# Kernel tuning notes

Hardware: AMD Instinct MI355X
Metric: run time of the kernel (lower is better)

Reference implementation:

```python
import jax, jax.numpy as jnp
import numpy as np

T_LEN, E_LEN, BATCH, DIM = 32, 256, 16, 512  # topic_len, exp_len, batch, input=hidden size
HID = 512


def setup_inputs() -> dict:
    key = jax.random.key(0)
    k1, k2, k3, k4, k5, k6 = jax.random.split(key, 6)
    topic = jax.random.normal(k1, (T_LEN, BATCH, DIM), dtype=jnp.float32)
    exp_output = jax.random.normal(k2, (E_LEN, BATCH, DIM), dtype=jnp.float32)
    seq_mask = jax.random.bernoulli(k3, 0.1, (E_LEN, BATCH))  # True = masked exp position
    # nn.Linear(hidden+input, hidden): weight [HID, HID+DIM], bias [HID]
    lim1 = 1.0 / np.sqrt(HID + DIM)
    W_attn = jax.random.uniform(k4, (HID, HID + DIM), minval=-lim1, maxval=lim1, dtype=jnp.float32)
    b_attn = jax.random.uniform(k5, (HID,), minval=-lim1, maxval=lim1, dtype=jnp.float32)
    # nn.Linear(hidden, 1): weight [1, HID], bias [1]
    lim2 = 1.0 / np.sqrt(HID)
    kv, kb = jax.random.split(k6)
    v_score = jax.random.uniform(kv, (1, HID), minval=-lim2, maxval=lim2, dtype=jnp.float32)
    b_score = jax.random.uniform(kb, (1,), minval=-lim2, maxval=lim2, dtype=jnp.float32)
    return {"topic": topic, "exp_output": exp_output, "seq_mask": seq_mask,
            "W_attn": W_attn, "b_attn": b_attn, "v_score": v_score, "b_score": b_score}


def reference(topic, exp_output, seq_mask, W_attn, b_attn, v_score, b_score):
    # topic: [T, B, D]; exp_output: [E, B, D]; seq_mask: [E, B] bool
    D = topic.shape[2]
    # Split the concat-Linear: cat(topic, exp) @ W.T == topic @ W[:, :D].T + exp @ W[:, D:].T
    proj_t = jnp.einsum('tbd,hd->bth', topic, W_attn[:, :D])        # [B, T, H]
    proj_e = jnp.einsum('ebd,hd->beh', exp_output, W_attn[:, D:])   # [B, E, H]
    feat = jnp.tanh(proj_t[:, :, None, :] + proj_e[:, None, :, :] + b_attn)  # [B, T, E, H]
    energies = jnp.einsum('bteh,h->bte', feat, v_score[0]) + b_score[0]      # [B, T, E]
    # mask exp positions (broadcast over topic dim), as masked_fill(-1e12)
    energies = jnp.where(seq_mask.T[:, None, :], jnp.float32(-1e12), energies)
    attn_s1 = jax.nn.softmax(jnp.swapaxes(energies, 1, 2), axis=2)  # [B, E, T], softmax over topics
    attn_s2 = jax.nn.softmax(energies, axis=2)                      # [B, T, E], softmax over exp
    new_exp = jnp.einsum('bet,btd->bed', attn_s1, jnp.swapaxes(topic, 0, 1))       # [B, E, D]
    new_topic = jnp.einsum('bte,bed->btd', attn_s2, jnp.swapaxes(exp_output, 0, 1))  # [B, T, D]
    return new_topic, new_exp
```

## Files before the change

### kernel.cpp

```cpp
#include <hip/hip_runtime.h>
#include <hip/hip_bf16.h>
#include <cstddef>
#include <cstdint>

#define T_LEN 32
#define E_LEN 256
#define BATCH 16
#define DIM 512
#define HID 512
#define WROW 1024

#define TWO_LOG2E 2.8853900817779268f
#define LOG2E 1.4426950408889634f

typedef __attribute__((ext_vector_type(8))) short bf16x8;
typedef __attribute__((ext_vector_type(4))) float f32x4;

__device__ inline bf16x8 cvt8(float4 a, float4 b) {
    union { bf16x8 v; __hip_bfloat16 h[8]; } u;
    u.h[0] = __float2bfloat16(a.x); u.h[1] = __float2bfloat16(a.y);
    u.h[2] = __float2bfloat16(a.z); u.h[3] = __float2bfloat16(a.w);
    u.h[4] = __float2bfloat16(b.x); u.h[5] = __float2bfloat16(b.y);
    u.h[6] = __float2bfloat16(b.z); u.h[7] = __float2bfloat16(b.w);
    return u.v;
}

#define GPAD 8
#define GLDR (64 + GPAD)

__global__ __launch_bounds__(256) void gemm_fused_k(
    const float* __restrict__ topic, const float* __restrict__ expo,
    const float* __restrict__ W, const float* __restrict__ battn,
    float* __restrict__ EPT, __hip_bfloat16* __restrict__ EPE) {
    __shared__ __align__(16) __hip_bfloat16 As[2][64 * GLDR];
    __shared__ __align__(16) __hip_bfloat16 Bs[2][64 * GLDR];
    const int tid = threadIdx.x;
    const int by = blockIdx.x >> 3;
    const int n0 = (blockIdx.x & 7) * 64;
    const float* A; const float* Wp; int m0;
    const bool isT = (by < 8);
    if (isT) { A = topic; Wp = W;       m0 = by * 64; }
    else     { A = expo;  Wp = W + DIM; m0 = (by - 8) * 64; }
    const int w = tid >> 6;
    const int lane = tid & 63;
    const int l15 = lane & 15;
    const int g = lane >> 4;
    const int srow = tid >> 2;
    const int sc = tid & 3;

    f32x4 acc[4];
    const f32x4 z = {0.f, 0.f, 0.f, 0.f};
#pragma unroll
    for (int nt = 0; nt < 4; ++nt) acc[nt] = z;

    const float* ga = A + (size_t)(m0 + srow) * 512 + sc * 8;
    const float* gb = Wp + (size_t)(n0 + srow) * WROW + sc * 8;

    float4 a0 = *(const float4*)(ga);
    float4 a1 = *(const float4*)(ga + 4);
    float4 a2 = *(const float4*)(ga + 32);
    float4 a3 = *(const float4*)(ga + 36);
    float4 b0 = *(const float4*)(gb);
    float4 b1 = *(const float4*)(gb + 4);
    float4 b2 = *(const float4*)(gb + 32);
    float4 b3 = *(const float4*)(gb + 36);

    for (int kk = 0; kk < 8; ++kk) {
        const int cur = kk & 1;
        bf16x8 av0 = cvt8(a0, a1), av1 = cvt8(a2, a3);
        bf16x8 bv0 = cvt8(b0, b1), bv1 = cvt8(b2, b3);
        if (kk < 7) {
            ga += 64; gb += 64;
            a0 = *(const float4*)(ga);
            a1 = *(const float4*)(ga + 4);
            a2 = *(const float4*)(ga + 32);
            a3 = *(const float4*)(ga + 36);
            b0 = *(const float4*)(gb);
            b1 = *(const float4*)(gb + 4);
            b2 = *(const float4*)(gb + 32);
            b3 = *(const float4*)(gb + 36);
        }
        *(bf16x8*)&As[cur][srow * GLDR + sc * 8] = av0;
        *(bf16x8*)&As[cur][srow * GLDR + sc * 8 + 32] = av1;
        *(bf16x8*)&Bs[cur][srow * GLDR + sc * 8] = bv0;
        *(bf16x8*)&Bs[cur][srow * GLDR + sc * 8 + 32] = bv1;
        __syncthreads();
#pragma unroll
        for (int s = 0; s < 2; ++s) {
            bf16x8 af = *(const bf16x8*)&As[cur][(w * 16 + l15) * GLDR + (s * 4 + g) * 8];
#pragma unroll
            for (int nt = 0; nt < 4; ++nt) {
                bf16x8 bf = *(const bf16x8*)&Bs[cur][(nt * 16 + l15) * GLDR + (s * 4 + g) * 8];
                acc[nt] = __builtin_amdgcn_mfma_f32_16x16x32_bf16(af, bf, acc[nt], 0, 0, 0);
            }
        }
    }
    if (isT) {
#pragma unroll
        for (int nt = 0; nt < 4; ++nt) {
            int n = n0 + nt * 16 + l15;
            float bv = battn[n];
#pragma unroll
            for (int r = 0; r < 4; ++r) {
                int m = m0 + w * 16 + g * 4 + r;
                EPT[(size_t)m * 512 + n] =
                    __builtin_amdgcn_exp2f((acc[nt][r] + bv) * TWO_LOG2E);
            }
        }
    } else {
#pragma unroll
        for (int nt = 0; nt < 4; ++nt) {
            int n = n0 + nt * 16 + l15;
#pragma unroll
            for (int r = 0; r < 4; ++r) {
                int m = m0 + w * 16 + g * 4 + r;
                EPE[(size_t)m * 512 + n] = __float2bfloat16(
                    __builtin_amdgcn_exp2f(acc[nt][r] * TWO_LOG2E));
            }
        }
    }
}

__global__ __launch_bounds__(256) void energies_k(
    const float* __restrict__ EPT, const __hip_bfloat16* __restrict__ EPE,
    const float* __restrict__ v, const int* __restrict__ mask,
    float* __restrict__ P, float* __restrict__ PT) {
    const int u = blockIdx.x;
    const int b = u & 15;
    const int tg = (u >> 4) & 3;
    const int ech = u >> 6;
    const int tid = threadIdx.x;
    const int lane = tid & 63;
    const int w = tid >> 6;
    const int h0 = lane * 8;
    const int e0 = ech * 16 + w * 4;
    const bool o1 = (lane & 1) != 0;
    const bool o2 = (lane & 2) != 0;
    const bool o4 = (lane & 4) != 0;

    int mk[4];
#pragma unroll
    for (int ei = 0; ei < 4; ++ei) mk[ei] = mask[(e0 + ei) * BATCH + b];

    float sv[8], sv2[4], spt[8][8];
    {
        float4 v0 = *(const float4*)(v + h0);
        float4 v1 = *(const float4*)(v + h0 + 4);
        sv[0] = -2.f * v0.x; sv[1] = -2.f * v0.y; sv[2] = -2.f * v0.z; sv[3] = -2.f * v0.w;
        sv[4] = -2.f * v1.x; sv[5] = -2.f * v1.y; sv[6] = -2.f * v1.z; sv[7] = -2.f * v1.w;
        sv2[0] = sv[0] + sv[1]; sv2[1] = sv[2] + sv[3];
        sv2[2] = sv[4] + sv[5]; sv2[3] = sv[6] + sv[7];
#pragma unroll
        for (int i = 0; i < 8; ++i) {
            const float* p = EPT + ((size_t)((tg * 8 + i) * BATCH + b)) * HID + h0;
            float4 p0 = *(const float4*)(p);
            float4 p1 = *(const float4*)(p + 4);
            spt[i][0] = p0.x; spt[i][1] = p0.y; spt[i][2] = p0.z; spt[i][3] = p0.w;
            spt[i][4] = p1.x; spt[i][5] = p1.y; spt[i][6] = p1.z; spt[i][7] = p1.w;
        }
    }
#pragma unroll
    for (int ei = 0; ei < 4; ++ei) {
        const int e = e0 + ei;
        if (mk[ei] != 0) {
            if (lane < 8) {
                P[((size_t)b * T_LEN + tg * 8 + lane) * E_LEN + e] = 1e-30f;
                PT[((size_t)b * E_LEN + e) * T_LEN + tg * 8 + lane] = 1e-30f;
            }
            continue;
        }
        union { bf16x8 v8; __hip_bfloat16 h[8]; } pv;
        pv.v8 = *(const bf16x8*)(EPE + ((size_t)(e * BATCH + b)) * HID + h0);
        float pr[8];
#pragma unroll
        for (int j = 0; j < 8; ++j) pr[j] = __bfloat162float(pv.h[j]);
        float a[8] = {0.f, 0.f, 0.f, 0.f, 0.f, 0.f, 0.f, 0.f};
#pragma unroll
        for (int i = 0; i < 8; ++i) {
#pragma unroll
            for (int jq = 0; jq < 2; ++jq) {
                const int j0 = jq * 4;
                float a0 = spt[i][j0 + 0] * pr[j0 + 0];
                float a1 = spt[i][j0 + 1] * pr[j0 + 1];
                float a2 = spt[i][j0 + 2] * pr[j0 + 2];
                float a3 = spt[i][j0 + 3] * pr[j0 + 3];
                float u0 = a0 + 1.0f;
                float u2 = a2 + 1.0f;
                float d01 = fmaf(a1, u0, u0);
                float d23 = fmaf(a3, u2, u2);
                float n01 = fmaf(sv[j0 + 0], a1, fmaf(sv[j0 + 1], a0, sv2[jq * 2 + 0]));
                float n23 = fmaf(sv[j0 + 2], a3, fmaf(sv[j0 + 3], a2, sv2[jq * 2 + 1]));
                float nn = fmaf(n01, d23, n23 * d01);
                float dd = d01 * d23;
                a[i] = fmaf(nn, __builtin_amdgcn_rcpf(dd), a[i]);
            }
        }
        float s, b0, b1, b2, b3, d0, d1, f;
        s = __shfl_xor(o1 ? a[0] : a[1], 1); b0 = (o1 ? a[1] : a[0]) + s;
        s = __shfl_xor(o1 ? a[2] : a[3], 1); b1 = (o1 ? a[3] : a[2]) + s;
        s = __shfl_xor(o1 ? a[4] : a[5], 1); b2 = (o1 ? a[5] : a[4]) + s;
        s = __shfl_xor(o1 ? a[6] : a[7], 1); b3 = (o1 ? a[7] : a[6]) + s;
        s = __shfl_xor(o2 ? b0 : b1, 2); d0 = (o2 ? b1 : b0) + s;
        s = __shfl_xor(o2 ? b2 : b3, 2); d1 = (o2 ? b3 : b2) + s;
        s = __shfl_xor(o4 ? d0 : d1, 4); f = (o4 ? d1 : d0) + s;
        f += __shfl_xor(f, 8);
        f += __shfl_xor(f, 16);
        f += __shfl_xor(f, 32);
        if (lane < 8) {
            float pe = __builtin_amdgcn_exp2f(f * LOG2E);
            P[((size_t)b * T_LEN + tg * 8 + lane) * E_LEN + e] = pe;
            PT[((size_t)b * E_LEN + e) * T_LEN + tg * 8 + lane] = pe;
        }
    }
}

__global__ __launch_bounds__(256) void epilogue_k(
    const float* __restrict__ P, const float* __restrict__ PT,
    const float* __restrict__ topic,
    const float* __restrict__ expo, float* __restrict__ out) {
    __shared__ __align__(16) float smem[5120];
    const int tid = threadIdx.x;
    const int lane = tid & 63;
    const int w = tid >> 6;
    if (blockIdx.x < 512) {
        const int b = blockIdx.x >> 5;
        const int ech = (blockIdx.x >> 1) & 15;
        const int hf = blockIdx.x & 1;
        const int e0 = ech * 16 + w * 4;
#pragma unroll
        for (int ei = 0; ei < 4; ++ei) {
            const int e = e0 + ei;
            float x = 0.f;
            if (lane < T_LEN)
                x = PT[((size_t)b * E_LEN + e) * T_LEN + lane];
            float s = x;
#pragma unroll
            for (int off = 32; off; off >>= 1) s += __shfl_xor(s, off);
            float wv = x * __builtin_amdgcn_rcpf(s);
            if (lane < T_LEN) smem[(w * 4 + ei) * 32 + lane] = wv;
        }
        __syncthreads();
        const int d0 = hf * 256 + lane * 4;
        float4 acc[4];
#pragma unroll
        for (int ei = 0; ei < 4; ++ei) acc[ei] = {0.f, 0.f, 0.f, 0.f};
#pragma unroll 2
        for (int tq = 0; tq < 8; ++tq) {
            float wqa[4][4];
#pragma unroll
            for (int ei = 0; ei < 4; ++ei) {
                float4 q = *(const float4*)&smem[(w * 4 + ei) * 32 + tq * 4];
                wqa[ei][0] = q.x; wqa[ei][1] = q.y; wqa[ei][2] = q.z; wqa[ei][3] = q.w;
            }
#pragma unroll
            for (int tt = 0; tt < 4; ++tt) {
                const int t = tq * 4 + tt;
                float4 r = *(const float4*)(topic + ((size_t)t * BATCH + b) * DIM + d0);
#pragma unroll
                for (int ei = 0; ei < 4; ++ei) {
                    acc[ei].x = fmaf(wqa[ei][tt], r.x, acc[ei].x);
                    acc[ei].y = fmaf(wqa[ei][tt], r.y, acc[ei].y);
                    acc[ei].z = fmaf(wqa[ei][tt], r.z, acc[ei].z);
                    acc[ei].w = fmaf(wqa[ei][tt], r.w, acc[ei].w);
                }
            }
        }
#pragma unroll
        for (int ei = 0; ei < 4; ++ei) {
            float* o = out + (size_t)BATCH * T_LEN * DIM +
                       ((size_t)b * E_LEN + e0 + ei) * DIM + d0;
            *(float4*)o = acc[ei];
        }
    } else {
        const int q = blockIdx.x - 512;
        const int b = q >> 4;
        const int tq = (q >> 1) & 7;
        const int hf = q & 1;
        {
            const int bt = b * T_LEN + tq * 4 + w;
            float4 xv = *(const float4*)&P[(size_t)bt * E_LEN + lane * 4];
            float s = xv.x + xv.y + xv.z + xv.w;
#pragma unroll
            for (int off = 32; off; off >>= 1) s += __shfl_xor(s, off);
            float inv = __builtin_amdgcn_rcpf(s);
            smem[(lane * 4 + 0) * 4 + w] = xv.x * inv;
            smem[(lane * 4 + 1) * 4 + w] = xv.y * inv;
            smem[(lane * 4 + 2) * 4 + w] = xv.z * inv;
            smem[(lane * 4 + 3) * 4 + w] = xv.w * inv;
        }
        __syncthreads();
        const int dl = lane * 4;
        const int dglob = hf * 256 + dl;
        float4 a0 = {0.f, 0.f, 0.f, 0.f};
        float4 a1 = {0.f, 0.f, 0.f, 0.f};
        float4 a2 = {0.f, 0.f, 0.f, 0.f};
        float4 a3 = {0.f, 0.f, 0.f, 0.f};
        const float* base = expo + (size_t)b * DIM + dglob;
        for (int ee = 0; ee < 64; ++ee) {
            const int e = w * 64 + ee;
            float4 rv = *(const float4*)(base + (size_t)e * BATCH * DIM);
            float4 wq = *(const float4*)&smem[e * 4];
            a0.x = fmaf(wq.x, rv.x, a0.x); a0.y = fmaf(wq.x, rv.y, a0.y);
            a0.z = fmaf(wq.x, rv.z, a0.z); a0.w = fmaf(wq.x, rv.w, a0.w);
            a1.x = fmaf(wq.y, rv.x, a1.x); a1.y = fmaf(wq.y, rv.y, a1.y);
            a1.z = fmaf(wq.y, rv.z, a1.z); a1.w = fmaf(wq.y, rv.w, a1.w);
            a2.x = fmaf(wq.z, rv.x, a2.x); a2.y = fmaf(wq.z, rv.y, a2.y);
            a2.z = fmaf(wq.z, rv.z, a2.z); a2.w = fmaf(wq.z, rv.w, a2.w);
            a3.x = fmaf(wq.w, rv.x, a3.x); a3.y = fmaf(wq.w, rv.y, a3.y);
            a3.z = fmaf(wq.w, rv.z, a3.z); a3.w = fmaf(wq.w, rv.w, a3.w);
        }
        *(float4*)&smem[1024 + (w * 4 + 0) * 256 + dl] = a0;
        *(float4*)&smem[1024 + (w * 4 + 1) * 256 + dl] = a1;
        *(float4*)&smem[1024 + (w * 4 + 2) * 256 + dl] = a2;
        *(float4*)&smem[1024 + (w * 4 + 3) * 256 + dl] = a3;
        __syncthreads();
#pragma unroll
        for (int tt = 0; tt < 4; ++tt) {
            float sum = smem[1024 + (0 * 4 + tt) * 256 + tid] +
                        smem[1024 + (1 * 4 + tt) * 256 + tid] +
                        smem[1024 + (2 * 4 + tt) * 256 + tid] +
                        smem[1024 + (3 * 4 + tt) * 256 + tid];
            out[((size_t)b * T_LEN + tq * 4 + tt) * DIM + hf * 256 + tid] = sum;
        }
    }
}

extern "C" void kernel_launch(void* const* d_in, const int* in_sizes, int n_in,
                              void* d_out, int out_size, void* d_ws, size_t ws_size,
                              hipStream_t stream) {
    const float* topic = (const float*)d_in[0];
    const float* expo  = (const float*)d_in[1];
    const int*   mask  = (const int*)d_in[2];
    const float* W     = (const float*)d_in[3];
    const float* battn = (const float*)d_in[4];
    const float* vsc   = (const float*)d_in[5];
    float* out = (float*)d_out;

    float* EPT = (float*)d_ws;
    __hip_bfloat16* EPE = (__hip_bfloat16*)(EPT + 512 * 512);
    float* P  = (float*)(EPE + (size_t)4096 * 512);
    float* PT = P + (size_t)BATCH * T_LEN * E_LEN;

    gemm_fused_k<<<576, 256, 0, stream>>>(topic, expo, W, battn, EPT, EPE);
    energies_k<<<1024, 256, 0, stream>>>(EPT, EPE, vsc, mask, P, PT);
    epilogue_k<<<768, 256, 0, stream>>>(P, PT, topic, expo, out);
}
```

Before: 111.2 us.

## Fuse topic-softmax and new_exp computation into energies kernel via LDS

The energies kernel now assigns each block all 32 topics for 8 exp positions of one batch, loops over topic chunks, and keeps the exp weights in LDS. It then normalizes over topics and computes new_exp directly, which removes the PT transposed buffer and its global round trip. The new_topic part becomes its own smaller kernel. In exchange the grid drops from 1024 to 512 blocks and EPT rows are reloaded per topic chunk, which may lower parallelism.

```diff
diff --git a/kernel.cpp b/kernel.cpp
--- a/kernel.cpp
+++ b/kernel.cpp
@@ -121,28 +121,29 @@
     }
 }
 
-__global__ __launch_bounds__(256) void energies_k(
+__global__ __launch_bounds__(256) void energies_exp_k(
     const float* __restrict__ EPT, const __hip_bfloat16* __restrict__ EPE,
     const float* __restrict__ v, const int* __restrict__ mask,
-    float* __restrict__ P, float* __restrict__ PT) {
+    const float* __restrict__ topic, float* __restrict__ P,
+    float* __restrict__ out) {
+    __shared__ __align__(16) float P_lds[8][32];
     const int u = blockIdx.x;
-    const int b = u & 15;
-    const int tg = (u >> 4) & 3;
-    const int ech = u >> 6;
+    const int b = u >> 5;
+    const int ech = u & 31;
     const int tid = threadIdx.x;
     const int lane = tid & 63;
     const int w = tid >> 6;
     const int h0 = lane * 8;
-    const int e0 = ech * 16 + w * 4;
+    const int e0 = ech * 8 + w * 2;
     const bool o1 = (lane & 1) != 0;
     const bool o2 = (lane & 2) != 0;
     const bool o4 = (lane & 4) != 0;
 
-    int mk[4];
-#pragma unroll
-    for (int ei = 0; ei < 4; ++ei) mk[ei] = mask[(e0 + ei) * BATCH + b];
-
-    float sv[8], sv2[4], spt[8][8];
+    int mk[2];
+    mk[0] = mask[(e0 + 0) * BATCH + b];
+    mk[1] = mask[(e0 + 1) * BATCH + b];
+
+    float sv[8], sv2[4];
     {
         float4 v0 = *(const float4*)(v + h0);
         float4 v1 = *(const float4*)(v + h0 + 4);
@@ -150,178 +151,183 @@
         sv[4] = -2.f * v1.x; sv[5] = -2.f * v1.y; sv[6] = -2.f * v1.z; sv[7] = -2.f * v1.w;
         sv2[0] = sv[0] + sv[1]; sv2[1] = sv[2] + sv[3];
         sv2[2] = sv[4] + sv[5]; sv2[3] = sv[6] + sv[7];
+    }
+    float pr2[2][8];
+#pragma unroll
+    for (int ei = 0; ei < 2; ++ei) {
+        if (mk[ei] == 0) {
+            union { bf16x8 v8; __hip_bfloat16 h[8]; } pv;
+            pv.v8 = *(const bf16x8*)(EPE + ((size_t)((e0 + ei) * BATCH + b)) * HID + h0);
+#pragma unroll
+            for (int j = 0; j < 8; ++j) pr2[ei][j] = __bfloat162float(pv.h[j]);
+        }
+    }
+
+    for (int tc = 0; tc < 4; ++tc) {
+        float spt[8][8];
 #pragma unroll
         for (int i = 0; i < 8; ++i) {
-            const float* p = EPT + ((size_t)((tg * 8 + i) * BATCH + b)) * HID + h0;
+            const float* p = EPT + ((size_t)((tc * 8 + i) * BATCH + b)) * HID + h0;
             float4 p0 = *(const float4*)(p);
             float4 p1 = *(const float4*)(p + 4);
             spt[i][0] = p0.x; spt[i][1] = p0.y; spt[i][2] = p0.z; spt[i][3] = p0.w;
             spt[i][4] = p1.x; spt[i][5] = p1.y; spt[i][6] = p1.z; spt[i][7] = p1.w;
         }
-    }
-#pragma unroll
-    for (int ei = 0; ei < 4; ++ei) {
-        const int e = e0 + ei;
-        if (mk[ei] != 0) {
+#pragma unroll
+        for (int ei = 0; ei < 2; ++ei) {
+            const int e = e0 + ei;
+            if (mk[ei] != 0) {
+                if (lane < 8) {
+                    P[((size_t)b * T_LEN + tc * 8 + lane) * E_LEN + e] = 1e-30f;
+                    P_lds[w * 2 + ei][tc * 8 + lane] = 1e-30f;
+                }
+                continue;
+            }
+            float a[8] = {0.f, 0.f, 0.f, 0.f, 0.f, 0.f, 0.f, 0.f};
+#pragma unroll
+            for (int i = 0; i < 8; ++i) {
+#pragma unroll
+                for (int jq = 0; jq < 2; ++jq) {
+                    const int j0 = jq * 4;
+                    float a0 = spt[i][j0 + 0] * pr2[ei][j0 + 0];
+                    float a1 = spt[i][j0 + 1] * pr2[ei][j0 + 1];
+                    float a2 = spt[i][j0 + 2] * pr2[ei][j0 + 2];
+                    float a3 = spt[i][j0 + 3] * pr2[ei][j0 + 3];
+                    float u0 = a0 + 1.0f;
+                    float u2 = a2 + 1.0f;
+                    float d01 = fmaf(a1, u0, u0);
+                    float d23 = fmaf(a3, u2, u2);
+                    float n01 = fmaf(sv[j0 + 0], a1, fmaf(sv[j0 + 1], a0, sv2[jq * 2 + 0]));
+                    float n23 = fmaf(sv[j0 + 2], a3, fmaf(sv[j0 + 3], a2, sv2[jq * 2 + 1]));
+                    float nn = fmaf(n01, d23, n23 * d01);
+                    float dd = d01 * d23;
+                    a[i] = fmaf(nn, __builtin_amdgcn_rcpf(dd), a[i]);
+                }
+            }
+            float s, b0, b1, b2, b3, d0, d1, f;
+            s = __shfl_xor(o1 ? a[0] : a[1], 1); b0 = (o1 ? a[1] : a[0]) + s;
+            s = __shfl_xor(o1 ? a[2] : a[3], 1); b1 = (o1 ? a[3] : a[2]) + s;
+            s = __shfl_xor(o1 ? a[4] : a[5], 1); b2 = (o1 ? a[5] : a[4]) + s;
+            s = __shfl_xor(o1 ? a[6] : a[7], 1); b3 = (o1 ? a[7] : a[6]) + s;
+            s = __shfl_xor(o2 ? b0 : b1, 2); d0 = (o2 ? b1 : b0) + s;
+            s = __shfl_xor(o2 ? b2 : b3, 2); d1 = (o2 ? b3 : b2) + s;
+            s = __shfl_xor(o4 ? d0 : d1, 4); f = (o4 ? d1 : d0) + s;
+            f += __shfl_xor(f, 8);
+            f += __shfl_xor(f, 16);
+            f += __shfl_xor(f, 32);
             if (lane < 8) {
-                P[((size_t)b * T_LEN + tg * 8 + lane) * E_LEN + e] = 1e-30f;
-                PT[((size_t)b * E_LEN + e) * T_LEN + tg * 8 + lane] = 1e-30f;
-            }
-            continue;
-        }
-        union { bf16x8 v8; __hip_bfloat16 h[8]; } pv;
-        pv.v8 = *(const bf16x8*)(EPE + ((size_t)(e * BATCH + b)) * HID + h0);
-        float pr[8];
-#pragma unroll
-        for (int j = 0; j < 8; ++j) pr[j] = __bfloat162float(pv.h[j]);
-        float a[8] = {0.f, 0.f, 0.f, 0.f, 0.f, 0.f, 0.f, 0.f};
-#pragma unroll
-        for (int i = 0; i < 8; ++i) {
-#pragma unroll
-            for (int jq = 0; jq < 2; ++jq) {
-                const int j0 = jq * 4;
-                float a0 = spt[i][j0 + 0] * pr[j0 + 0];
-                float a1 = spt[i][j0 + 1] * pr[j0 + 1];
-                float a2 = spt[i][j0 + 2] * pr[j0 + 2];
-                float a3 = spt[i][j0 + 3] * pr[j0 + 3];
-                float u0 = a0 + 1.0f;
-                float u2 = a2 + 1.0f;
-                float d01 = fmaf(a1, u0, u0);
-                float d23 = fmaf(a3, u2, u2);
-                float n01 = fmaf(sv[j0 + 0], a1, fmaf(sv[j0 + 1], a0, sv2[jq * 2 + 0]));
-                float n23 = fmaf(sv[j0 + 2], a3, fmaf(sv[j0 + 3], a2, sv2[jq * 2 + 1]));
-                float nn = fmaf(n01, d23, n23 * d01);
-                float dd = d01 * d23;
-                a[i] = fmaf(nn, __builtin_amdgcn_rcpf(dd), a[i]);
-            }
-        }
-        float s, b0, b1, b2, b3, d0, d1, f;
-        s = __shfl_xor(o1 ? a[0] : a[1], 1); b0 = (o1 ? a[1] : a[0]) + s;
-        s = __shfl_xor(o1 ? a[2] : a[3], 1); b1 = (o1 ? a[3] : a[2]) + s;
-        s = __shfl_xor(o1 ? a[4] : a[5], 1); b2 = (o1 ? a[5] : a[4]) + s;
-        s = __shfl_xor(o1 ? a[6] : a[7], 1); b3 = (o1 ? a[7] : a[6]) + s;
-        s = __shfl_xor(o2 ? b0 : b1, 2); d0 = (o2 ? b1 : b0) + s;
-        s = __shfl_xor(o2 ? b2 : b3, 2); d1 = (o2 ? b3 : b2) + s;
-        s = __shfl_xor(o4 ? d0 : d1, 4); f = (o4 ? d1 : d0) + s;
-        f += __shfl_xor(f, 8);
-        f += __shfl_xor(f, 16);
-        f += __shfl_xor(f, 32);
-        if (lane < 8) {
-            float pe = __builtin_amdgcn_exp2f(f * LOG2E);
-            P[((size_t)b * T_LEN + tg * 8 + lane) * E_LEN + e] = pe;
-            PT[((size_t)b * E_LEN + e) * T_LEN + tg * 8 + lane] = pe;
-        }
-    }
-}
-
-__global__ __launch_bounds__(256) void epilogue_k(
-    const float* __restrict__ P, const float* __restrict__ PT,
-    const float* __restrict__ topic,
-    const float* __restrict__ expo, float* __restrict__ out) {
+                float pe = __builtin_amdgcn_exp2f(f * LOG2E);
+                P[((size_t)b * T_LEN + tc * 8 + lane) * E_LEN + e] = pe;
+                P_lds[w * 2 + ei][tc * 8 + lane] = pe;
+            }
+        }
+    }
+    __syncthreads();
+
+    const int el0 = w * 2, el1 = w * 2 + 1;
+    float s0 = 0.f, s1 = 0.f;
+#pragma unroll
+    for (int q = 0; q < 8; ++q) {
+        float4 x = *(const float4*)&P_lds[el0][q * 4];
+        s0 += (x.x + x.y) + (x.z + x.w);
+        float4 y = *(const float4*)&P_lds[el1][q * 4];
+        s1 += (y.x + y.y) + (y.z + y.w);
+    }
+    const float inv0 = __builtin_amdgcn_rcpf(s0);
+    const float inv1 = __builtin_amdgcn_rcpf(s1);
+
+    const int dA = lane * 4;
+    const int dB = 256 + lane * 4;
+    float4 aA0 = {0.f, 0.f, 0.f, 0.f}, aB0 = {0.f, 0.f, 0.f, 0.f};
+    float4 aA1 = {0.f, 0.f, 0.f, 0.f}, aB1 = {0.f, 0.f, 0.f, 0.f};
+#pragma unroll 2
+    for (int tq = 0; tq < 8; ++tq) {
+        float4 w0 = *(const float4*)&P_lds[el0][tq * 4];
+        float4 w1 = *(const float4*)&P_lds[el1][tq * 4];
+        w0.x *= inv0; w0.y *= inv0; w0.z *= inv0; w0.w *= inv0;
+        w1.x *= inv1; w1.y *= inv1; w1.z *= inv1; w1.w *= inv1;
+        float wt0[4] = {w0.x, w0.y, w0.z, w0.w};
+        float wt1[4] = {w1.x, w1.y, w1.z, w1.w};
+#pragma unroll
+        for (int tt = 0; tt < 4; ++tt) {
+            const int t = tq * 4 + tt;
+            const float* tp = topic + ((size_t)t * BATCH + b) * DIM;
+            float4 rA = *(const float4*)(tp + dA);
+            float4 rB = *(const float4*)(tp + dB);
+            aA0.x = fmaf(wt0[tt], rA.x, aA0.x); aA0.y = fmaf(wt0[tt], rA.y, aA0.y);
+            aA0.z = fmaf(wt0[tt], rA.z, aA0.z); aA0.w = fmaf(wt0[tt], rA.w, aA0.w);
+            aB0.x = fmaf(wt0[tt], rB.x, aB0.x); aB0.y = fmaf(wt0[tt], rB.y, aB0.y);
+            aB0.z = fmaf(wt0[tt], rB.z, aB0.z); aB0.w = fmaf(wt0[tt], rB.w, aB0.w);
+            aA1.x = fmaf(wt1[tt], rA.x, aA1.x); aA1.y = fmaf(wt1[tt], rA.y, aA1.y);
+            aA1.z = fmaf(wt1[tt], rA.z, aA1.z); aA1.w = fmaf(wt1[tt], rA.w, aA1.w);
+            aB1.x = fmaf(wt1[tt], rB.x, aB1.x); aB1.y = fmaf(wt1[tt], rB.y, aB1.y);
+            aB1.z = fmaf(wt1[tt], rB.z, aB1.z); aB1.w = fmaf(wt1[tt], rB.w, aB1.w);
+        }
+    }
+    float* oe0 = out + (size_t)BATCH * T_LEN * DIM + ((size_t)b * E_LEN + e0) * DIM;
+    *(float4*)(oe0 + dA) = aA0;
+    *(float4*)(oe0 + dB) = aB0;
+    float* oe1 = oe0 + DIM;
+    *(float4*)(oe1 + dA) = aA1;
+    *(float4*)(oe1 + dB) = aB1;
+}
+
+__global__ __launch_bounds__(256) void newtopic_k(
+    const float* __restrict__ P, const float* __restrict__ expo,
+    float* __restrict__ out) {
     __shared__ __align__(16) float smem[5120];
     const int tid = threadIdx.x;
     const int lane = tid & 63;
     const int w = tid >> 6;
-    if (blockIdx.x < 512) {
-        const int b = blockIdx.x >> 5;
-        const int ech = (blockIdx.x >> 1) & 15;
-        const int hf = blockIdx.x & 1;
-        const int e0 = ech * 16 + w * 4;
-#pragma unroll
-        for (int ei = 0; ei < 4; ++ei) {
-            const int e = e0 + ei;
-            float x = 0.f;
-            if (lane < T_LEN)
-                x = PT[((size_t)b * E_LEN + e) * T_LEN + lane];
-            float s = x;
-#pragma unroll
-            for (int off = 32; off; off >>= 1) s += __shfl_xor(s, off);
-            float wv = x * __builtin_amdgcn_rcpf(s);
-            if (lane < T_LEN) smem[(w * 4 + ei) * 32 + lane] = wv;
-        }
-        __syncthreads();
-        const int d0 = hf * 256 + lane * 4;
-        float4 acc[4];
-#pragma unroll
-        for (int ei = 0; ei < 4; ++ei) acc[ei] = {0.f, 0.f, 0.f, 0.f};
-#pragma unroll 2
-        for (int tq = 0; tq < 8; ++tq) {
-            float wqa[4][4];
-#pragma unroll
-            for (int ei = 0; ei < 4; ++ei) {
-                float4 q = *(const float4*)&smem[(w * 4 + ei) * 32 + tq * 4];
-                wqa[ei][0] = q.x; wqa[ei][1] = q.y; wqa[ei][2] = q.z; wqa[ei][3] = q.w;
-            }
-#pragma unroll
-            for (int tt = 0; tt < 4; ++tt) {
-                const int t = tq * 4 + tt;
-                float4 r = *(const float4*)(topic + ((size_t)t * BATCH + b) * DIM + d0);
-#pragma unroll
-                for (int ei = 0; ei < 4; ++ei) {
-                    acc[ei].x = fmaf(wqa[ei][tt], r.x, acc[ei].x);
-                    acc[ei].y = fmaf(wqa[ei][tt], r.y, acc[ei].y);
-                    acc[ei].z = fmaf(wqa[ei][tt], r.z, acc[ei].z);
-                    acc[ei].w = fmaf(wqa[ei][tt], r.w, acc[ei].w);
-                }
-            }
-        }
-#pragma unroll
-        for (int ei = 0; ei < 4; ++ei) {
-            float* o = out + (size_t)BATCH * T_LEN * DIM +
-                       ((size_t)b * E_LEN + e0 + ei) * DIM + d0;
-            *(float4*)o = acc[ei];
-        }
-    } else {
-        const int q = blockIdx.x - 512;
-        const int b = q >> 4;
-        const int tq = (q >> 1) & 7;
-        const int hf = q & 1;
-        {
-            const int bt = b * T_LEN + tq * 4 + w;
-            float4 xv = *(const float4*)&P[(size_t)bt * E_LEN + lane * 4];
-            float s = xv.x + xv.y + xv.z + xv.w;
-#pragma unroll
-            for (int off = 32; off; off >>= 1) s += __shfl_xor(s, off);
-            float inv = __builtin_amdgcn_rcpf(s);
-            smem[(lane * 4 + 0) * 4 + w] = xv.x * inv;
-            smem[(lane * 4 + 1) * 4 + w] = xv.y * inv;
-            smem[(lane * 4 + 2) * 4 + w] = xv.z * inv;
-            smem[(lane * 4 + 3) * 4 + w] = xv.w * inv;
-        }
-        __syncthreads();
-        const int dl = lane * 4;
-        const int dglob = hf * 256 + dl;
-        float4 a0 = {0.f, 0.f, 0.f, 0.f};
-        float4 a1 = {0.f, 0.f, 0.f, 0.f};
-        float4 a2 = {0.f, 0.f, 0.f, 0.f};
-        float4 a3 = {0.f, 0.f, 0.f, 0.f};
-        const float* base = expo + (size_t)b * DIM + dglob;
-        for (int ee = 0; ee < 64; ++ee) {
-            const int e = w * 64 + ee;
-            float4 rv = *(const float4*)(base + (size_t)e * BATCH * DIM);
-            float4 wq = *(const float4*)&smem[e * 4];
-            a0.x = fmaf(wq.x, rv.x, a0.x); a0.y = fmaf(wq.x, rv.y, a0.y);
-            a0.z = fmaf(wq.x, rv.z, a0.z); a0.w = fmaf(wq.x, rv.w, a0.w);
-            a1.x = fmaf(wq.y, rv.x, a1.x); a1.y = fmaf(wq.y, rv.y, a1.y);
-            a1.z = fmaf(wq.y, rv.z, a1.z); a1.w = fmaf(wq.y, rv.w, a1.w);
-            a2.x = fmaf(wq.z, rv.x, a2.x); a2.y = fmaf(wq.z, rv.y, a2.y);
-            a2.z = fmaf(wq.z, rv.z, a2.z); a2.w = fmaf(wq.z, rv.w, a2.w);
-            a3.x = fmaf(wq.w, rv.x, a3.x); a3.y = fmaf(wq.w, rv.y, a3.y);
-            a3.z = fmaf(wq.w, rv.z, a3.z); a3.w = fmaf(wq.w, rv.w, a3.w);
-        }
-        *(float4*)&smem[1024 + (w * 4 + 0) * 256 + dl] = a0;
-        *(float4*)&smem[1024 + (w * 4 + 1) * 256 + dl] = a1;
-        *(float4*)&smem[1024 + (w * 4 + 2) * 256 + dl] = a2;
-        *(float4*)&smem[1024 + (w * 4 + 3) * 256 + dl] = a3;
-        __syncthreads();
-#pragma unroll
-        for (int tt = 0; tt < 4; ++tt) {
-            float sum = smem[1024 + (0 * 4 + tt) * 256 + tid] +
-                        smem[1024 + (1 * 4 + tt) * 256 + tid] +
-                        smem[1024 + (2 * 4 + tt) * 256 + tid] +
-                        smem[1024 + (3 * 4 + tt) * 256 + tid];
-            out[((size_t)b * T_LEN + tq * 4 + tt) * DIM + hf * 256 + tid] = sum;
-        }
+    const int q = blockIdx.x;
+    const int b = q >> 4;
+    const int tq = (q >> 1) & 7;
+    const int hf = q & 1;
+    {
+        const int bt = b * T_LEN + tq * 4 + w;
+        float4 xv = *(const float4*)&P[(size_t)bt * E_LEN + lane * 4];
+        float s = xv.x + xv.y + xv.z + xv.w;
+#pragma unroll
+        for (int off = 32; off; off >>= 1) s += __shfl_xor(s, off);
+        float inv = __builtin_amdgcn_rcpf(s);
+        smem[(lane * 4 + 0) * 4 + w] = xv.x * inv;
+        smem[(lane * 4 + 1) * 4 + w] = xv.y * inv;
+        smem[(lane * 4 + 2) * 4 + w] = xv.z * inv;
+        smem[(lane * 4 + 3) * 4 + w] = xv.w * inv;
+    }
+    __syncthreads();
+    const int dl = lane * 4;
+    const int dglob = hf * 256 + dl;
+    float4 a0 = {0.f, 0.f, 0.f, 0.f};
+    float4 a1 = {0.f, 0.f, 0.f, 0.f};
+    float4 a2 = {0.f, 0.f, 0.f, 0.f};
+    float4 a3 = {0.f, 0.f, 0.f, 0.f};
+    const float* base = expo + (size_t)b * DIM + dglob;
+    for (int ee = 0; ee < 64; ++ee) {
+        const int e = w * 64 + ee;
+        float4 rv = *(const float4*)(base + (size_t)e * BATCH * DIM);
+        float4 wq = *(const float4*)&smem[e * 4];
+        a0.x = fmaf(wq.x, rv.x, a0.x); a0.y = fmaf(wq.x, rv.y, a0.y);
+        a0.z = fmaf(wq.x, rv.z, a0.z); a0.w = fmaf(wq.x, rv.w, a0.w);
+        a1.x = fmaf(wq.y, rv.x, a1.x); a1.y = fmaf(wq.y, rv.y, a1.y);
+        a1.z = fmaf(wq.y, rv.z, a1.z); a1.w = fmaf(wq.y, rv.w, a1.w);
+        a2.x = fmaf(wq.z, rv.x, a2.x); a2.y = fmaf(wq.z, rv.y, a2.y);
+        a2.z = fmaf(wq.z, rv.z, a2.z); a2.w = fmaf(wq.z, rv.w, a2.w);
+        a3.x = fmaf(wq.w, rv.x, a3.x); a3.y = fmaf(wq.w, rv.y, a3.y);
+        a3.z = fmaf(wq.w, rv.z, a3.z); a3.w = fmaf(wq.w, rv.w, a3.w);
+    }
+    *(float4*)&smem[1024 + (w * 4 + 0) * 256 + dl] = a0;
+    *(float4*)&smem[1024 + (w * 4 + 1) * 256 + dl] = a1;
+    *(float4*)&smem[1024 + (w * 4 + 2) * 256 + dl] = a2;
+    *(float4*)&smem[1024 + (w * 4 + 3) * 256 + dl] = a3;
+    __syncthreads();
+#pragma unroll
+    for (int tt = 0; tt < 4; ++tt) {
+        float sum = smem[1024 + (0 * 4 + tt) * 256 + tid] +
+                    smem[1024 + (1 * 4 + tt) * 256 + tid] +
+                    smem[1024 + (2 * 4 + tt) * 256 + tid] +
+                    smem[1024 + (3 * 4 + tt) * 256 + tid];
+        out[((size_t)b * T_LEN + tq * 4 + tt) * DIM + hf * 256 + tid] = sum;
     }
 }
 
@@ -338,10 +344,9 @@
 
     float* EPT = (float*)d_ws;
     __hip_bfloat16* EPE = (__hip_bfloat16*)(EPT + 512 * 512);
-    float* P  = (float*)(EPE + (size_t)4096 * 512);
-    float* PT = P + (size_t)BATCH * T_LEN * E_LEN;
+    float* P = (float*)(EPE + (size_t)4096 * 512);
 
     gemm_fused_k<<<576, 256, 0, stream>>>(topic, expo, W, battn, EPT, EPE);
-    energies_k<<<1024, 256, 0, stream>>>(EPT, EPE, vsc, mask, P, PT);
-    epilogue_k<<<768, 256, 0, stream>>>(P, PT, topic, expo, out);
-}
+    energies_exp_k<<<512, 256, 0, stream>>>(EPT, EPE, vsc, mask, topic, P, out);
+    newtopic_k<<<256, 256, 0, stream>>>(P, expo, out);
+}
```

Measured after the change: 113.8 us. 2.4% more time.
